# Optimization experiments

Hardware: AMD Instinct MI355X
Metric: run time of the kernel (lower is better)

Reference implementation:

```python
import jax, jax.numpy as jnp
import numpy as np

B = 1024
D = 512
M = 65536          # num_memory
C = 4096           # num pseudo-label clusters (= labels.max()+1, fixed for jit)
TEMP = 0.05
EPS = 1e-6


def setup_inputs() -> dict:
    key = jax.random.key(0)
    k1, k2, k3, k4 = jax.random.split(key, 4)
    inputs = jax.random.normal(k1, (B, D), dtype=jnp.float32)
    indexes = jax.random.randint(k2, (B,), 0, M, dtype=jnp.int64)
    feats = jax.random.normal(k3, (M, D), dtype=jnp.float32)
    # memory bank stores L2-normalized features (see _update_feature)
    features = feats / jnp.linalg.norm(feats, axis=1, keepdims=True)
    labels = jax.random.randint(k4, (M,), 0, C, dtype=jnp.int64)
    return {"inputs": inputs, "indexes": indexes, "features": features, "labels": labels}


def reference(inputs, indexes, features, labels):
    # F.normalize(inputs, p=2, dim=1)
    x = inputs / jnp.linalg.norm(inputs, axis=1, keepdims=True)
    # HM.forward: inputs @ features.T, then / temp  -> sim over memory slots [B, M]
    sim = (x @ features.T) / TEMP
    # index_add over labels: per-cluster sum of sim columns  -> [C, B]
    sim_c = jax.ops.segment_sum(sim.T, labels, num_segments=C)
    nums = jax.ops.segment_sum(jnp.ones((M,), dtype=sim.dtype), labels, num_segments=C)  # [C]
    cluster_mask = (nums > 0).astype(sim.dtype)                     # [C]
    # mean within cluster; empty clusters divide by 1
    avg = sim_c / jnp.where(nums > 0, nums, 1.0)[:, None]           # [C, B]
    # masked_softmax over clusters, per sample
    vec = avg.T                                                     # [B, C]
    masked_exps = jnp.exp(vec) * cluster_mask[None, :]
    probs = masked_exps / (jnp.sum(masked_exps, axis=1, keepdims=True) + EPS)
    # F.nll_loss(log(probs + eps), targets) with targets = labels[indexes]
    targets = labels[indexes]                                       # [B]
    logp = jnp.log(probs + EPS)
    loss = -jnp.mean(logp[jnp.arange(B), targets])
    return loss
```

## Files before the change

kernel.cpp:

```cpp
#include <hip/hip_runtime.h>
#include <hip/hip_bf16.h>

#define NB 1024
#define ND 512
#define NM 65536
#define NC 4096
#define CAP 128

static constexpr float TEMP = 0.05f;
static constexpr float EPSF = 1e-6f;

typedef __attribute__((ext_vector_type(8))) short short8v;
typedef __attribute__((ext_vector_type(16))) float f32x16;

static __device__ __forceinline__ short f2bf(float f) {
    __hip_bfloat16 h = __float2bfloat16(f);
    return *reinterpret_cast<short*>(&h);
}

__global__ __launch_bounds__(256) void k_init(const int* __restrict__ indexes,
                                              const int* __restrict__ labels,
                                              int* __restrict__ cnt,
                                              float* __restrict__ denom,
                                              int* __restrict__ tgt,
                                              int* __restrict__ flag) {
    int i = blockIdx.x * 256 + threadIdx.x;
    if (i < NC) cnt[i] = 0;
    else if (i < NC + NB) denom[i - NC] = 0.f;
    else if (i < NC + 2 * NB) { int b = i - NC - NB; tgt[b] = labels[indexes[b]]; }
    else if (i == NC + 2 * NB) flag[0] = 0;
}

__global__ __launch_bounds__(512) void k_norm_scatter(const float* __restrict__ in,
                                                      const int* __restrict__ labels,
                                                      short* __restrict__ xnb,
                                                      int* __restrict__ cnt,
                                                      int* __restrict__ idx) {
    const int b = blockIdx.x;
    const int wid = threadIdx.x >> 6, l = threadIdx.x & 63;
    if (wid < 4) {
        int row = b * 4 + wid;
        const float4* rp = reinterpret_cast<const float4*>(in + (size_t)row * ND) + l * 2;
        float4 v0 = rp[0], v1 = rp[1];
        float ss = v0.x * v0.x + v0.y * v0.y + v0.z * v0.z + v0.w * v0.w
                 + v1.x * v1.x + v1.y * v1.y + v1.z * v1.z + v1.w * v1.w;
#pragma unroll
        for (int m = 1; m < 64; m <<= 1) ss += __shfl_xor(ss, m);
        float inv = 1.0f / sqrtf(ss);
        short8v o;
        o[0] = f2bf(v0.x * inv); o[1] = f2bf(v0.y * inv);
        o[2] = f2bf(v0.z * inv); o[3] = f2bf(v0.w * inv);
        o[4] = f2bf(v1.x * inv); o[5] = f2bf(v1.y * inv);
        o[6] = f2bf(v1.z * inv); o[7] = f2bf(v1.w * inv);
        *reinterpret_cast<short8v*>(xnb + (size_t)row * ND + l * 8) = o;
    } else {
        int m = b * 256 + (threadIdx.x - 256);
        int c = labels[m];
        int pos = atomicAdd(&cnt[c], 1);
        if (pos < CAP) idx[(size_t)c * CAP + pos] = m;
    }
}

__global__ __launch_bounds__(128) void k_gather(const float* __restrict__ feats,
                                                const int* __restrict__ idx,
                                                const int* __restrict__ cnt,
                                                short* __restrict__ Gb) {
    int c = blockIdx.x;
    int t = threadIdx.x;
    int n = cnt[c];
    if (n > CAP) n = CAP;
    const int* bucket = idx + (size_t)c * CAP;
    const float4* F = reinterpret_cast<const float4*>(feats);
    float4 a0 = {0.f, 0.f, 0.f, 0.f}, a1 = {0.f, 0.f, 0.f, 0.f};
    float4 a2 = {0.f, 0.f, 0.f, 0.f}, a3 = {0.f, 0.f, 0.f, 0.f};
    int j = 0;
    for (; j + 3 < n; j += 4) {
        int m0 = bucket[j], m1 = bucket[j + 1];
        int m2 = bucket[j + 2], m3 = bucket[j + 3];
        float4 v0 = F[(size_t)m0 * 128 + t];
        float4 v1 = F[(size_t)m1 * 128 + t];
        float4 v2 = F[(size_t)m2 * 128 + t];
        float4 v3 = F[(size_t)m3 * 128 + t];
        a0.x += v0.x; a0.y += v0.y; a0.z += v0.z; a0.w += v0.w;
        a1.x += v1.x; a1.y += v1.y; a1.z += v1.z; a1.w += v1.w;
        a2.x += v2.x; a2.y += v2.y; a2.z += v2.z; a2.w += v2.w;
        a3.x += v3.x; a3.y += v3.y; a3.z += v3.z; a3.w += v3.w;
    }
    for (; j < n; ++j) {
        int m0 = bucket[j];
        float4 v0 = F[(size_t)m0 * 128 + t];
        a0.x += v0.x; a0.y += v0.y; a0.z += v0.z; a0.w += v0.w;
    }
    short4 o;
    o.x = f2bf(a0.x + a1.x + a2.x + a3.x);
    o.y = f2bf(a0.y + a1.y + a2.y + a3.y);
    o.z = f2bf(a0.z + a1.z + a2.z + a3.z);
    o.w = f2bf(a0.w + a1.w + a2.w + a3.w);
    reinterpret_cast<short4*>(Gb + (size_t)c * ND)[t] = o;
}

__global__ __launch_bounds__(256) void k_gemm_final(const short* __restrict__ A,
                                                    const short* __restrict__ Bm,
                                                    const int* __restrict__ cnt,
                                                    const int* __restrict__ tgt,
                                                    float* __restrict__ denom,
                                                    float* __restrict__ numer,
                                                    int* __restrict__ flag,
                                                    float* __restrict__ out) {
    const int tid = threadIdx.x;
    const int w = tid >> 6;
    const int lane = tid & 63;
    const int ln = lane & 31;
    const int kg = lane >> 5;
    const int row0 = blockIdx.y * 128 + (w >> 1) * 64;
    const int col0 = blockIdx.x * 128 + (w & 1) * 64;

    f32x16 acc00 = {}, acc01 = {}, acc10 = {}, acc11 = {};
    const short* pa0 = A + (size_t)(row0 + ln) * ND + kg * 8;
    const short* pa1 = pa0 + 32 * ND;
    const short* pb0 = Bm + (size_t)(col0 + ln) * ND + kg * 8;
    const short* pb1 = pb0 + 32 * ND;
#pragma unroll 8
    for (int k0 = 0; k0 < ND; k0 += 16) {
        short8v a0 = *reinterpret_cast<const short8v*>(pa0 + k0);
        short8v a1 = *reinterpret_cast<const short8v*>(pa1 + k0);
        short8v b0 = *reinterpret_cast<const short8v*>(pb0 + k0);
        short8v b1 = *reinterpret_cast<const short8v*>(pb1 + k0);
        acc00 = __builtin_amdgcn_mfma_f32_32x32x16_bf16(a0, b0, acc00, 0, 0, 0);
        acc01 = __builtin_amdgcn_mfma_f32_32x32x16_bf16(a0, b1, acc01, 0, 0, 0);
        acc10 = __builtin_amdgcn_mfma_f32_32x32x16_bf16(a1, b0, acc10, 0, 0, 0);
        acc11 = __builtin_amdgcn_mfma_f32_32x32x16_bf16(a1, b1, acc11, 0, 0, 0);
    }
    int colA = col0 + ln;
    int colB = colA + 32;
    int nA = cnt[colA], nB = cnt[colB];
    float invA = 1.0f / (TEMP * (float)(nA > 0 ? nA : 1));
    float invB = 1.0f / (TEMP * (float)(nB > 0 ? nB : 1));
    float mA = (nA > 0) ? 1.f : 0.f;
    float mB = (nB > 0) ? 1.f : 0.f;
    int rbase = row0 + 4 * kg;
#pragma unroll
    for (int r = 0; r < 16; ++r) {
        int row = rbase + (r & 3) + 8 * (r >> 2);
        int rowH = row + 32;
        float v00 = acc00[r] * invA, v01 = acc01[r] * invB;
        float v10 = acc10[r] * invA, v11 = acc11[r] * invB;
        int t0 = tgt[row], t1 = tgt[rowH];
        if (t0 == colA) numer[row] = v00;
        if (t0 == colB) numer[row] = v01;
        if (t1 == colA) numer[rowH] = v10;
        if (t1 == colB) numer[rowH] = v11;
        float s0 = mA * __expf(v00) + mB * __expf(v01);
        float s1 = mA * __expf(v10) + mB * __expf(v11);
#pragma unroll
        for (int m = 1; m < 32; m <<= 1) {
            s0 += __shfl_xor(s0, m);
            s1 += __shfl_xor(s1, m);
        }
        if (ln == 0) {
            atomicAdd(&denom[row], s0);
            atomicAdd(&denom[rowH], s1);
        }
    }

    __syncthreads();
    if (tid == 0) {
        __threadfence();
        atomicAdd(flag, 1);
    }
    if (blockIdx.x != 0 || blockIdx.y != 0) return;

    if (tid == 0) {
        while (atomicAdd(flag, 0) < 256) __builtin_amdgcn_s_sleep(8);
        __threadfence();
    }
    __syncthreads();
    float s = 0.f;
    for (int i = tid; i < NB; i += 256) {
        float p = __expf(numer[i]) / (denom[i] + EPSF);
        s += -logf(p + EPSF);
    }
#pragma unroll
    for (int o = 32; o > 0; o >>= 1) s += __shfl_down(s, o);
    __shared__ float sw[4];
    if (lane == 0) sw[w] = s;
    __syncthreads();
    if (tid == 0) out[0] = (sw[0] + sw[1] + sw[2] + sw[3]) / (float)NB;
}

extern "C" void kernel_launch(void* const* d_in, const int* in_sizes, int n_in,
                              void* d_out, int out_size, void* d_ws, size_t ws_size,
                              hipStream_t stream) {
    const float* inputs   = (const float*)d_in[0];
    const int*   indexes  = (const int*)d_in[1];
    const float* features = (const float*)d_in[2];
    const int*   labels   = (const int*)d_in[3];
    float* out = (float*)d_out;

    short* Gb     = (short*)d_ws;
    short* xnb    = Gb + (size_t)NC * ND;
    float* denom  = (float*)(xnb + (size_t)NB * ND);
    float* numer  = denom + NB;
    int*   tgt    = (int*)(numer + NB);
    int*   flag   = tgt + NB;
    int*   cnt    = flag + 64;
    int*   idx    = cnt + NC;

    k_init<<<25, 256, 0, stream>>>(indexes, labels, cnt, denom, tgt, flag);
    k_norm_scatter<<<NB / 4, 512, 0, stream>>>(inputs, labels, xnb, cnt, idx);
    k_gather<<<NC, 128, 0, stream>>>(features, idx, cnt, Gb);
    dim3 g(NC / 128, NB / 128);
    k_gemm_final<<<g, 256, 0, stream>>>(xnb, Gb, cnt, tgt, denom, numer, flag, out);
}
```

Baseline: 75.62 us.

## Fuse gather and GEMM with per-column-tile flags; split final reduction kernel

Merges the cluster gather and the GEMM into one launch. The first 2048 blocks each gather two clusters and bump a per-column-tile flag, and the GEMM blocks spin on the flag for their column tile so they can start as soon as their 128 clusters are ready. Zeroing of counters and denominators moves into the normalisation kernel, the label scatter becomes its own kernel, and the final loss reduction is a separate single-block kernel instead of a spin-wait inside the GEMM. This trades launch gaps and the global barrier for spin-waiting blocks, which could deadlock or stall if GEMM blocks occupy compute units before the gather blocks are scheduled.

```diff
diff --git a/kernel.cpp b/kernel.cpp
--- a/kernel.cpp
+++ b/kernel.cpp
@@ -18,107 +18,118 @@
     return *reinterpret_cast<short*>(&h);
 }
 
-__global__ __launch_bounds__(256) void k_init(const int* __restrict__ indexes,
-                                              const int* __restrict__ labels,
-                                              int* __restrict__ cnt,
-                                              float* __restrict__ denom,
-                                              int* __restrict__ tgt,
-                                              int* __restrict__ flag) {
-    int i = blockIdx.x * 256 + threadIdx.x;
-    if (i < NC) cnt[i] = 0;
-    else if (i < NC + NB) denom[i - NC] = 0.f;
-    else if (i < NC + 2 * NB) { int b = i - NC - NB; tgt[b] = labels[indexes[b]]; }
-    else if (i == NC + 2 * NB) flag[0] = 0;
-}
-
-__global__ __launch_bounds__(512) void k_norm_scatter(const float* __restrict__ in,
-                                                      const int* __restrict__ labels,
-                                                      short* __restrict__ xnb,
-                                                      int* __restrict__ cnt,
-                                                      int* __restrict__ idx) {
-    const int b = blockIdx.x;
-    const int wid = threadIdx.x >> 6, l = threadIdx.x & 63;
-    if (wid < 4) {
-        int row = b * 4 + wid;
-        const float4* rp = reinterpret_cast<const float4*>(in + (size_t)row * ND) + l * 2;
-        float4 v0 = rp[0], v1 = rp[1];
-        float ss = v0.x * v0.x + v0.y * v0.y + v0.z * v0.z + v0.w * v0.w
-                 + v1.x * v1.x + v1.y * v1.y + v1.z * v1.z + v1.w * v1.w;
-#pragma unroll
-        for (int m = 1; m < 64; m <<= 1) ss += __shfl_xor(ss, m);
-        float inv = 1.0f / sqrtf(ss);
-        short8v o;
-        o[0] = f2bf(v0.x * inv); o[1] = f2bf(v0.y * inv);
-        o[2] = f2bf(v0.z * inv); o[3] = f2bf(v0.w * inv);
-        o[4] = f2bf(v1.x * inv); o[5] = f2bf(v1.y * inv);
-        o[6] = f2bf(v1.z * inv); o[7] = f2bf(v1.w * inv);
-        *reinterpret_cast<short8v*>(xnb + (size_t)row * ND + l * 8) = o;
-    } else {
-        int m = b * 256 + (threadIdx.x - 256);
-        int c = labels[m];
-        int pos = atomicAdd(&cnt[c], 1);
-        if (pos < CAP) idx[(size_t)c * CAP + pos] = m;
-    }
-}
-
-__global__ __launch_bounds__(128) void k_gather(const float* __restrict__ feats,
-                                                const int* __restrict__ idx,
-                                                const int* __restrict__ cnt,
-                                                short* __restrict__ Gb) {
-    int c = blockIdx.x;
-    int t = threadIdx.x;
-    int n = cnt[c];
-    if (n > CAP) n = CAP;
-    const int* bucket = idx + (size_t)c * CAP;
-    const float4* F = reinterpret_cast<const float4*>(feats);
-    float4 a0 = {0.f, 0.f, 0.f, 0.f}, a1 = {0.f, 0.f, 0.f, 0.f};
-    float4 a2 = {0.f, 0.f, 0.f, 0.f}, a3 = {0.f, 0.f, 0.f, 0.f};
-    int j = 0;
-    for (; j + 3 < n; j += 4) {
-        int m0 = bucket[j], m1 = bucket[j + 1];
-        int m2 = bucket[j + 2], m3 = bucket[j + 3];
-        float4 v0 = F[(size_t)m0 * 128 + t];
-        float4 v1 = F[(size_t)m1 * 128 + t];
-        float4 v2 = F[(size_t)m2 * 128 + t];
-        float4 v3 = F[(size_t)m3 * 128 + t];
-        a0.x += v0.x; a0.y += v0.y; a0.z += v0.z; a0.w += v0.w;
-        a1.x += v1.x; a1.y += v1.y; a1.z += v1.z; a1.w += v1.w;
-        a2.x += v2.x; a2.y += v2.y; a2.z += v2.z; a2.w += v2.w;
-        a3.x += v3.x; a3.y += v3.y; a3.z += v3.z; a3.w += v3.w;
-    }
-    for (; j < n; ++j) {
-        int m0 = bucket[j];
-        float4 v0 = F[(size_t)m0 * 128 + t];
-        a0.x += v0.x; a0.y += v0.y; a0.z += v0.z; a0.w += v0.w;
-    }
-    short4 o;
-    o.x = f2bf(a0.x + a1.x + a2.x + a3.x);
-    o.y = f2bf(a0.y + a1.y + a2.y + a3.y);
-    o.z = f2bf(a0.z + a1.z + a2.z + a3.z);
-    o.w = f2bf(a0.w + a1.w + a2.w + a3.w);
-    reinterpret_cast<short4*>(Gb + (size_t)c * ND)[t] = o;
-}
-
-__global__ __launch_bounds__(256) void k_gemm_final(const short* __restrict__ A,
-                                                    const short* __restrict__ Bm,
-                                                    const int* __restrict__ cnt,
-                                                    const int* __restrict__ tgt,
-                                                    float* __restrict__ denom,
-                                                    float* __restrict__ numer,
-                                                    int* __restrict__ flag,
-                                                    float* __restrict__ out) {
+__global__ __launch_bounds__(256) void k_norm_init(const float* __restrict__ in,
+                                                   const int* __restrict__ indexes,
+                                                   const int* __restrict__ labels,
+                                                   short* __restrict__ xnb,
+                                                   int* __restrict__ tgt,
+                                                   float* __restrict__ denom,
+                                                   int* __restrict__ cnt,
+                                                   int* __restrict__ flags) {
+    int wid = threadIdx.x >> 6, l = threadIdx.x & 63;
+    int b = blockIdx.x * 4 + wid;
+    const float4* row = reinterpret_cast<const float4*>(in + (size_t)b * ND) + l * 2;
+    float4 v0 = row[0], v1 = row[1];
+    float ss = v0.x * v0.x + v0.y * v0.y + v0.z * v0.z + v0.w * v0.w
+             + v1.x * v1.x + v1.y * v1.y + v1.z * v1.z + v1.w * v1.w;
+#pragma unroll
+    for (int m = 1; m < 64; m <<= 1) ss += __shfl_xor(ss, m);
+    float inv = 1.0f / sqrtf(ss);
+    short8v o;
+    o[0] = f2bf(v0.x * inv); o[1] = f2bf(v0.y * inv);
+    o[2] = f2bf(v0.z * inv); o[3] = f2bf(v0.w * inv);
+    o[4] = f2bf(v1.x * inv); o[5] = f2bf(v1.y * inv);
+    o[6] = f2bf(v1.z * inv); o[7] = f2bf(v1.w * inv);
+    *reinterpret_cast<short8v*>(xnb + (size_t)b * ND + l * 8) = o;
+    if (threadIdx.x < 16) cnt[blockIdx.x * 16 + threadIdx.x] = 0;
+    if (blockIdx.x == 0 && threadIdx.x < 32) flags[threadIdx.x] = 0;
+    if (l == 0) {
+        tgt[b] = labels[indexes[b]];
+        denom[b] = 0.f;
+    }
+}
+
+__global__ __launch_bounds__(256) void k_scatter(const int* __restrict__ labels,
+                                                 int* __restrict__ cnt,
+                                                 int* __restrict__ idx) {
+    int m = blockIdx.x * 256 + threadIdx.x;
+    int c = labels[m];
+    int pos = atomicAdd(&cnt[c], 1);
+    if (pos < CAP) idx[(size_t)c * CAP + pos] = m;
+}
+
+__global__ __launch_bounds__(256) void k_gather_gemm(const float* __restrict__ feats,
+                                                     const int* __restrict__ idx,
+                                                     const int* __restrict__ cnt,
+                                                     const short* __restrict__ xnb,
+                                                     short* __restrict__ Gb,
+                                                     const int* __restrict__ tgt,
+                                                     float* __restrict__ denom,
+                                                     float* __restrict__ numer,
+                                                     int* __restrict__ flags) {
+    const int bid = blockIdx.x;
     const int tid = threadIdx.x;
+
+    if (bid < 2048) {
+        int c = bid * 2 + (tid >> 7);
+        int col = tid & 127;
+        int n = cnt[c];
+        if (n > CAP) n = CAP;
+        const int* bucket = idx + (size_t)c * CAP;
+        const float4* F = reinterpret_cast<const float4*>(feats);
+        float4 a0 = {0.f, 0.f, 0.f, 0.f}, a1 = {0.f, 0.f, 0.f, 0.f};
+        float4 a2 = {0.f, 0.f, 0.f, 0.f}, a3 = {0.f, 0.f, 0.f, 0.f};
+        int j = 0;
+        for (; j + 3 < n; j += 4) {
+            int m0 = bucket[j], m1 = bucket[j + 1];
+            int m2 = bucket[j + 2], m3 = bucket[j + 3];
+            float4 v0 = F[(size_t)m0 * 128 + col];
+            float4 v1 = F[(size_t)m1 * 128 + col];
+            float4 v2 = F[(size_t)m2 * 128 + col];
+            float4 v3 = F[(size_t)m3 * 128 + col];
+            a0.x += v0.x; a0.y += v0.y; a0.z += v0.z; a0.w += v0.w;
+            a1.x += v1.x; a1.y += v1.y; a1.z += v1.z; a1.w += v1.w;
+            a2.x += v2.x; a2.y += v2.y; a2.z += v2.z; a2.w += v2.w;
+            a3.x += v3.x; a3.y += v3.y; a3.z += v3.z; a3.w += v3.w;
+        }
+        for (; j < n; ++j) {
+            int m0 = bucket[j];
+            float4 v0 = F[(size_t)m0 * 128 + col];
+            a0.x += v0.x; a0.y += v0.y; a0.z += v0.z; a0.w += v0.w;
+        }
+        short4 o;
+        o.x = f2bf(a0.x + a1.x + a2.x + a3.x);
+        o.y = f2bf(a0.y + a1.y + a2.y + a3.y);
+        o.z = f2bf(a0.z + a1.z + a2.z + a3.z);
+        o.w = f2bf(a0.w + a1.w + a2.w + a3.w);
+        reinterpret_cast<short4*>(Gb + (size_t)c * ND)[col] = o;
+        __syncthreads();
+        if (tid == 0) {
+            __threadfence();
+            atomicAdd(&flags[bid >> 6], 1);
+        }
+        return;
+    }
+
+    const int gb = bid - 2048;
+    const int bx = gb & 31, by = gb >> 5;
+    if (tid == 0) {
+        while (atomicAdd(&flags[bx], 0) < 64) __builtin_amdgcn_s_sleep(8);
+        __threadfence();
+    }
+    __syncthreads();
+
     const int w = tid >> 6;
     const int lane = tid & 63;
     const int ln = lane & 31;
     const int kg = lane >> 5;
-    const int row0 = blockIdx.y * 128 + (w >> 1) * 64;
-    const int col0 = blockIdx.x * 128 + (w & 1) * 64;
+    const int row0 = by * 128 + (w >> 1) * 64;
+    const int col0 = bx * 128 + (w & 1) * 64;
 
     f32x16 acc00 = {}, acc01 = {}, acc10 = {}, acc11 = {};
-    const short* pa0 = A + (size_t)(row0 + ln) * ND + kg * 8;
+    const short* pa0 = xnb + (size_t)(row0 + ln) * ND + kg * 8;
     const short* pa1 = pa0 + 32 * ND;
-    const short* pb0 = Bm + (size_t)(col0 + ln) * ND + kg * 8;
+    const short* pb0 = Gb + (size_t)(col0 + ln) * ND + kg * 8;
     const short* pb1 = pb0 + 32 * ND;
 #pragma unroll 8
     for (int k0 = 0; k0 < ND; k0 += 16) {
@@ -162,30 +173,23 @@
             atomicAdd(&denom[rowH], s1);
         }
     }
-
-    __syncthreads();
-    if (tid == 0) {
-        __threadfence();
-        atomicAdd(flag, 1);
-    }
-    if (blockIdx.x != 0 || blockIdx.y != 0) return;
-
-    if (tid == 0) {
-        while (atomicAdd(flag, 0) < 256) __builtin_amdgcn_s_sleep(8);
-        __threadfence();
-    }
-    __syncthreads();
+}
+
+__global__ __launch_bounds__(256) void k_final(const float* __restrict__ numer,
+                                               const float* __restrict__ denom,
+                                               float* __restrict__ out) {
     float s = 0.f;
-    for (int i = tid; i < NB; i += 256) {
+    for (int i = threadIdx.x; i < NB; i += 256) {
         float p = __expf(numer[i]) / (denom[i] + EPSF);
         s += -logf(p + EPSF);
     }
 #pragma unroll
     for (int o = 32; o > 0; o >>= 1) s += __shfl_down(s, o);
     __shared__ float sw[4];
+    int lane = threadIdx.x & 63, w = threadIdx.x >> 6;
     if (lane == 0) sw[w] = s;
     __syncthreads();
-    if (tid == 0) out[0] = (sw[0] + sw[1] + sw[2] + sw[3]) / (float)NB;
+    if (threadIdx.x == 0) out[0] = (sw[0] + sw[1] + sw[2] + sw[3]) / (float)NB;
 }
 
 extern "C" void kernel_launch(void* const* d_in, const int* in_sizes, int n_in,
@@ -202,13 +206,13 @@
     float* denom  = (float*)(xnb + (size_t)NB * ND);
     float* numer  = denom + NB;
     int*   tgt    = (int*)(numer + NB);
-    int*   flag   = tgt + NB;
-    int*   cnt    = flag + 64;
+    int*   flags  = tgt + NB;
+    int*   cnt    = flags + 64;
     int*   idx    = cnt + NC;
 
-    k_init<<<25, 256, 0, stream>>>(indexes, labels, cnt, denom, tgt, flag);
-    k_norm_scatter<<<NB / 4, 512, 0, stream>>>(inputs, labels, xnb, cnt, idx);
-    k_gather<<<NC, 128, 0, stream>>>(features, idx, cnt, Gb);
-    dim3 g(NC / 128, NB / 128);
-    k_gemm_final<<<g, 256, 0, stream>>>(xnb, Gb, cnt, tgt, denom, numer, flag, out);
-}
+    k_norm_init<<<NB / 4, 256, 0, stream>>>(inputs, indexes, labels, xnb, tgt, denom, cnt, flags);
+    k_scatter<<<NM / 256, 256, 0, stream>>>(labels, cnt, idx);
+    k_gather_gemm<<<2048 + 256, 256, 0, stream>>>(features, idx, cnt, xnb, Gb,
+                                                  tgt, denom, numer, flags);
+    k_final<<<1, 256, 0, stream>>>(numer, denom, out);
+}
```

New measurement: 201.8 us. +166.9%, slower.
